# Optimization experiments

Hardware: AMD Instinct MI355X
Metric: run time of the kernel (lower is better)

Reference implementation:

```python
import jax, jax.numpy as jnp
import numpy as np

B, I, J, C, H = 1, 384, 384, 128, 4
CH = 128          # overall hidden
HD = CH // H      # 32 per head
INF = 1000000000.0
EPS = 1e-5


def setup_inputs() -> dict:
    key = jax.random.key(0)
    ks = jax.random.split(key, 10)
    s = 0.02
    return {
        "x": jax.random.normal(ks[0], (B, I, J, C), dtype=jnp.float32),
        "mask": jnp.ones((B, I, J), dtype=jnp.float32),
        "ln_w": jnp.ones((C,), dtype=jnp.float32),
        "ln_b": jnp.zeros((C,), dtype=jnp.float32),
        "wz": jax.random.normal(ks[1], (C, H), dtype=jnp.float32) * s,
        "bz": jnp.zeros((H,), dtype=jnp.float32),
        "wq": jax.random.normal(ks[2], (C, CH), dtype=jnp.float32) * s,
        "wk": jax.random.normal(ks[3], (C, CH), dtype=jnp.float32) * s,
        "wv": jax.random.normal(ks[4], (C, CH), dtype=jnp.float32) * s,
        "wg": jax.random.normal(ks[5], (C, CH), dtype=jnp.float32) * s,
        "bg": jnp.ones((CH,), dtype=jnp.float32),
        "wo": jax.random.normal(ks[6], (CH, C), dtype=jnp.float32) * s,
        "bo": jnp.zeros((C,), dtype=jnp.float32),
    }


def _layer_norm(x, w, b):
    mu = jnp.mean(x, axis=-1, keepdims=True)
    var = jnp.mean(jnp.square(x - mu), axis=-1, keepdims=True)
    return (x - mu) * jax.lax.rsqrt(var + EPS) * w + b


def reference(x, mask, ln_w, ln_b, wz, bz, wq, wk, wv, wg, bg, wo, bo):
    # starting=True: attention over last row axis J
    x = _layer_norm(x, ln_w, ln_b)                      # [B,I,J,C]
    mask_bias = (INF * (mask - 1.0))[:, :, None, None, :]   # [B,I,1,1,J]
    # triangle bias: linear_z then permute (2,0,1), unsqueeze(-4) -> [B,1,H,I,J]
    tri_bias = jnp.einsum("bijc,ch->bhij", x, wz) + bz[None, :, None, None]
    tri_bias = tri_bias[:, None]                        # [B,1,H,I,J]

    q = jnp.einsum("bijc,cd->bijd", x, wq).reshape(B, I, J, H, HD)
    k = jnp.einsum("bijc,cd->bijd", x, wk).reshape(B, I, J, H, HD)
    v = jnp.einsum("bijc,cd->bijd", x, wv).reshape(B, I, J, H, HD)
    q = q / jnp.sqrt(jnp.float32(HD))

    a = jnp.einsum("biqhd,bikhd->bihqk", q, k)          # [B,I,H,J,J]
    a = a + mask_bias + tri_bias
    a = jax.nn.softmax(a, axis=-1)
    o = jnp.einsum("bihqk,bikhd->biqhd", a, v)          # [B,I,J,H,HD]

    g = jax.nn.sigmoid(jnp.einsum("bijc,cd->bijd", x, wg) + bg)
    o = o.reshape(B, I, J, CH) * g
    return jnp.einsum("bijd,dc->bijc", o, wo) + bo      # [B,I,J,C]
```

## Files before the change

### kernel.cpp

```cpp
#include <hip/hip_runtime.h>
#include <math.h>

#define I_DIM 384
#define C_DIM 128
#define H_NUM 4
#define HD_DIM 32
#define M_DIM (I_DIM*I_DIM)
#define INF_F 1000000000.0f
#define EPS_F 1e-5f
#define QSCALE 0.17677669529663687f
#define LOG2E_F 1.4426950408889634f

typedef __attribute__((ext_vector_type(8))) short short8;
typedef __attribute__((ext_vector_type(4))) float f32x4;
union U4S8 { uint4 u; short8 s; };

__device__ __forceinline__ unsigned short f2bf(float f) {
    unsigned int u = __float_as_uint(f);
    u += 0x7fffu + ((u >> 16) & 1u);
    return (unsigned short)(u >> 16);
}
__device__ __forceinline__ float bf2f(unsigned short h) {
    return __uint_as_float((unsigned int)h << 16);
}
__device__ __forceinline__ unsigned int pk2(float a, float b) {
    return (unsigned int)f2bf(a) | ((unsigned int)f2bf(b) << 16);
}
__device__ __forceinline__ unsigned int cvtpk(float lo, float hi) {
    unsigned int r;
    asm("v_cvt_pk_bf16_f32 %0, %1, %2" : "=v"(r) : "v"(lo), "v"(hi));
    return r;
}

__device__ uint4 wfmt_dev[5*4096];

__device__ __forceinline__ void load_lds16(const uint4* gp, void* lp) {
    __builtin_amdgcn_global_load_lds(
        (const __attribute__((address_space(1))) unsigned int*)gp,
        (__attribute__((address_space(3))) unsigned int*)lp,
        16, 0, 0);
}

__global__ __launch_bounds__(256) void wprep_kernel(
    const float* __restrict__ wq, const float* __restrict__ wk,
    const float* __restrict__ wg, const float* __restrict__ wv,
    const float* __restrict__ wo)
{
    const int tid  = blockIdx.x*256 + threadIdx.x;
    const int l    = tid & 63, tile = tid >> 6;
    const int ks   = tile & 3, nt = (tile >> 2) & 7;
    const int s    = (tile >> 5) & 1, m = tile >> 6;
    const float* W = (m==0)?wq:(m==1)?wk:(m==2)?wg:(m==3)?wv:wo;
    const float scale = (m==0) ? QSCALE*LOG2E_F : 1.f;
    const int n  = nt*16 + (l & 15);
    const int kb = ks*32 + (l >> 4)*8;
    unsigned int hw[4];
    #pragma unroll
    for (int jp = 0; jp < 4; ++jp) {
        unsigned short hs[2];
        #pragma unroll
        for (int e = 0; e < 2; ++e) {
            float v = W[(size_t)(kb + jp*2 + e)*C_DIM + n] * scale;
            unsigned short h = f2bf(v);
            if (s) h = f2bf(v - bf2f(h));
            hs[e] = h;
        }
        hw[jp] = (unsigned int)hs[0] | ((unsigned int)hs[1] << 16);
    }
    wfmt_dev[(size_t)m*4096 + (size_t)((s*8 + nt)*4 + ks)*64 + l] =
        make_uint4(hw[0], hw[1], hw[2], hw[3]);
}

__global__ __launch_bounds__(256, 3) void ln_proj_kernel(
    const float* __restrict__ x,
    const float* __restrict__ lnw, const float* __restrict__ lnb,
    const float* __restrict__ wz,  const float* __restrict__ bz,
    const float* __restrict__ bg,
    float* __restrict__ qo, unsigned short* __restrict__ ko16,
    unsigned int* __restrict__ vto, float* __restrict__ go,
    float* __restrict__ zo)
{
    __shared__ __align__(16) unsigned int xs[4096];
    __shared__ __align__(16) uint4 wbuf4[2048];
    unsigned int* vts = xs;

    const int t    = threadIdx.x;
    const int row0 = blockIdx.x * 64;
    const int w = t >> 6, l = t & 63, n16 = l & 15, quad = l >> 4;

    #pragma unroll
    for (int it = 0; it < 4; ++it) {
        const int tl = w*4 + it;
        const int s = tl >> 3, ntl = (tl >> 2) & 1, ks = tl & 3;
        load_lds16(wfmt_dev + (size_t)((s*8 + ntl)*4 + ks)*64 + l,
                   (char*)wbuf4 + tl*1024);
    }

    float4 xv[8];
    const int r = t >> 2, qt = t & 3, c0 = qt * 32;
    const int sw = (r & 7) << 2;
    {
        const float* xrow = x + (size_t)(row0 + r)*C_DIM + c0;
        float s = 0.f, ss = 0.f;
        #pragma unroll
        for (int i2 = 0; i2 < 8; i2++) {
            xv[i2] = ((const float4*)xrow)[i2];
            s  += xv[i2].x + xv[i2].y + xv[i2].z + xv[i2].w;
            ss += xv[i2].x*xv[i2].x + xv[i2].y*xv[i2].y
                + xv[i2].z*xv[i2].z + xv[i2].w*xv[i2].w;
        }
        s  += __shfl_xor(s, 1);  s  += __shfl_xor(s, 2);
        ss += __shfl_xor(ss, 1); ss += __shfl_xor(ss, 2);
        const float mean = s * (1.f/128.f);
        const float var  = ss * (1.f/128.f) - mean*mean;
        const float rstd = rsqrtf(var + EPS_F);
        const float4* wz4 = (const float4*)wz;
        float4 zacc = make_float4(0.f,0.f,0.f,0.f);
        #pragma unroll
        for (int i2 = 0; i2 < 8; i2++) {
            float4 w4 = ((const float4*)(lnw + c0))[i2];
            float4 b4 = ((const float4*)(lnb + c0))[i2];
            float4 r4;
            r4.x = (xv[i2].x - mean)*rstd*w4.x + b4.x;
            r4.y = (xv[i2].y - mean)*rstd*w4.y + b4.y;
            r4.z = (xv[i2].z - mean)*rstd*w4.z + b4.z;
            r4.w = (xv[i2].w - mean)*rstd*w4.w + b4.w;
            const float4 za = wz4[c0 + i2*4 + 0];
            const float4 zb_ = wz4[c0 + i2*4 + 1];
            const float4 zc = wz4[c0 + i2*4 + 2];
            const float4 zd = wz4[c0 + i2*4 + 3];
            zacc.x += r4.x*za.x + r4.y*zb_.x + r4.z*zc.x + r4.w*zd.x;
            zacc.y += r4.x*za.y + r4.y*zb_.y + r4.z*zc.y + r4.w*zd.y;
            zacc.z += r4.x*za.z + r4.y*zb_.z + r4.z*zc.z + r4.w*zd.z;
            zacc.w += r4.x*za.w + r4.y*zb_.w + r4.z*zc.w + r4.w*zd.w;
            const int wi = r*64 + qt*16 + i2*2;
            xs[(wi  ) ^ sw] = pk2(r4.x, r4.y);
            xs[(wi+1) ^ sw] = pk2(r4.z, r4.w);
            xv[i2] = r4;
        }
        zacc.x += __shfl_xor(zacc.x, 1); zacc.x += __shfl_xor(zacc.x, 2);
        zacc.y += __shfl_xor(zacc.y, 1); zacc.y += __shfl_xor(zacc.y, 2);
        zacc.z += __shfl_xor(zacc.z, 1); zacc.z += __shfl_xor(zacc.z, 2);
        zacc.w += __shfl_xor(zacc.w, 1); zacc.w += __shfl_xor(zacc.w, 2);
        const float zv = (qt==0)?zacc.x:(qt==1)?zacc.y:(qt==2)?zacc.z:zacc.w;
        zo[(size_t)qt*M_DIM + row0 + r] = (zv + bz[qt]) * LOG2E_F;
    }
    __syncthreads();

    U4S8 ah[4], al[4];
    const int arow = w*16 + n16;
    #pragma unroll
    for (int ks = 0; ks < 4; ++ks) {
        const int bofs = arow*256 + ((ks*64 + quad*16) ^ ((arow & 7) << 4));
        ah[ks].u = *(const uint4*)((const char*)xs + bofs);
    }
    __syncthreads();

    #pragma unroll
    for (int i2 = 0; i2 < 8; i2++) {
        const float4 r4 = xv[i2];
        const unsigned short h0 = f2bf(r4.x), h1 = f2bf(r4.y),
                             h2 = f2bf(r4.z), h3 = f2bf(r4.w);
        const int wi = r*64 + qt*16 + i2*2;
        xs[(wi  ) ^ sw] = (unsigned int)f2bf(r4.x - bf2f(h0))
                        | ((unsigned int)f2bf(r4.y - bf2f(h1)) << 16);
        xs[(wi+1) ^ sw] = (unsigned int)f2bf(r4.z - bf2f(h2))
                        | ((unsigned int)f2bf(r4.w - bf2f(h3)) << 16);
    }
    __syncthreads();
    #pragma unroll
    for (int ks = 0; ks < 4; ++ks) {
        const int bofs = arow*256 + ((ks*64 + quad*16) ^ ((arow & 7) << 4));
        al[ks].u = *(const uint4*)((const char*)xs + bofs);
    }

    const int i_blk = row0 / I_DIM;
    const int jp0   = (row0 % I_DIM) >> 1;
    const int rw0   = row0 + w*16 + quad*4;

    int p = 0;
    #pragma unroll
    for (int rd = 0; rd < 16; ++rd) {
        const int mi = rd >> 2, qq = rd & 3;

        if (rd < 15) {
            const int m2 = (rd+1) >> 2, q2 = (rd+1) & 3;
            #pragma unroll
            for (int it = 0; it < 4; ++it) {
                const int tl = w*4 + it;
                const int s = tl >> 3, ntl2 = (tl >> 2) & 1, ks = tl & 3;
                load_lds16(wfmt_dev + (size_t)m2*4096
                           + (size_t)((s*8 + (q2*2 + ntl2))*4 + ks)*64 + l,
                           (char*)wbuf4 + (p^1)*16384 + tl*1024);
            }
        }

        f32x4 acc[2];
        #pragma unroll
        for (int ntl = 0; ntl < 2; ++ntl) {
            f32x4 a = {0.f, 0.f, 0.f, 0.f};
            #pragma unroll
            for (int ks = 0; ks < 4; ++ks) {
                U4S8 bh, bl;
                bh.u = wbuf4[p*1024 + (    ntl*4 + ks)*64 + l];
                bl.u = wbuf4[p*1024 + (8 + ntl*4 + ks)*64 + l];
                a = __builtin_amdgcn_mfma_f32_16x16x32_bf16(ah[ks].s, bh.s, a, 0,0,0);
                a = __builtin_amdgcn_mfma_f32_16x16x32_bf16(al[ks].s, bh.s, a, 0,0,0);
                a = __builtin_amdgcn_mfma_f32_16x16x32_bf16(ah[ks].s, bl.s, a, 0,0,0);
            }
            acc[ntl] = a;
        }

        if (mi == 0) {
            #pragma unroll
            for (int ntl = 0; ntl < 2; ++ntl)
                #pragma unroll
                for (int rr = 0; rr < 4; ++rr)
                    qo[(size_t)(rw0 + rr)*C_DIM + qq*32 + ntl*16 + n16] =
                        acc[ntl][rr];
        } else if (mi == 1) {
            #pragma unroll
            for (int ntl = 0; ntl < 2; ++ntl)
                #pragma unroll
                for (int rr = 0; rr < 4; ++rr)
                    ko16[(size_t)(rw0 + rr)*C_DIM + qq*32 + ntl*16 + n16] =
                        f2bf(acc[ntl][rr]);
        } else if (mi == 2) {
            #pragma unroll
            for (int ntl = 0; ntl < 2; ++ntl) {
                const float bgv = bg[qq*32 + ntl*16 + n16];
                #pragma unroll
                for (int rr = 0; rr < 4; ++rr)
                    go[(size_t)(rw0 + rr)*C_DIM + qq*32 + ntl*16 + n16] =
                        1.f/(1.f + __expf(-(acc[ntl][rr] + bgv)));
            }
        } else {
            #pragma unroll
            for (int ntl = 0; ntl < 2; ++ntl)
                #pragma unroll
                for (int pr = 0; pr < 2; ++pr)
                    vts[(ntl*16 + n16)*33 + w*8 + quad*2 + pr] =
                        pk2(acc[ntl][2*pr], acc[ntl][2*pr+1]);
            __syncthreads();
            for (int idx = t; idx < 32*32; idx += 256) {
                const int ch_l = idx >> 5, pp = idx & 31;
                vto[((size_t)i_blk*C_DIM + qq*32 + ch_l)*192 + jp0 + pp] =
                    vts[ch_l*33 + pp];
            }
        }

        __syncthreads();
        p ^= 1;
    }
}

__global__ __launch_bounds__(256, 4) void attn_mfma_kernel(
    const float* q, const unsigned short* __restrict__ k16,
    const unsigned int* __restrict__ vt32, const float* __restrict__ zb,
    const float* __restrict__ mask, float* o)
{
    __shared__ uint4 VTf[24*64];
    __shared__ __align__(16) float mbl[384];

    const int ii = blockIdx.x;
    const int h  = blockIdx.y;
    const int t  = threadIdx.x;
    const size_t rbase = (size_t)ii*I_DIM*C_DIM + h*HD_DIM;

    for (int idx = t; idx < 1536; idx += 256) {
        const int d = idx / 48, m = idx - d*48;
        const int c = m / 12, rr = m - c*12;
        const int km = rr >> 2, qd = rr & 3;
        const int hh = d >> 4, nn = d & 15;
        const int f  = (c*3 + km)*2 + hh;
        const int l0 = qd*16 + nn;
        const int lp = l0 ^ ((l0 >> 3) & 7) ^ ((3*c + km) & 7);
        VTf[f*64 + lp] =
            ((const uint4*)vt32)[((size_t)ii*C_DIM + h*HD_DIM + d)*48 + m];
    }
    for (int jj = t; jj < 384; jj += 256)
        mbl[jj] = (INF_F*LOG2E_F) * (mask[(size_t)ii*I_DIM + jj] - 1.f);
    __syncthreads();

    const int w = t >> 6, l = t & 63;
    const int n16 = l & 15, quad = l >> 4;
    const int slA = n16 + ((quad & 1) << 5);
    const int slB = slA + 16;
    const bool hi = (quad & 2) != 0;
    const int lswz = l ^ ((l >> 3) & 7);
    const unsigned short* kf = k16 + rbase + (size_t)n16*C_DIM + quad*8;

    #pragma unroll 1
    for (int qt = 0; qt < 6; qt++) {
        const int qg = w*6 + qt;

        U4S8 a;
        {
            const float* qrow = q + rbase + (size_t)(qg*16 + n16)*C_DIM + quad*8;
            const float4 f0 = ((const float4*)qrow)[0];
            const float4 f1 = ((const float4*)qrow)[1];
            a.u = make_uint4(cvtpk(f0.x,f0.y), cvtpk(f0.z,f0.w),
                             cvtpk(f1.x,f1.y), cvtpk(f1.z,f1.w));
        }

        f32x4 oacc0 = {0.f,0.f,0.f,0.f}, oacc1 = {0.f,0.f,0.f,0.f};
        float lsum = 0.f;
        const float* zrow = zb + (size_t)h*M_DIM
                          + (size_t)(qg*16 + n16)*I_DIM + quad*4;

        #pragma unroll 1
        for (int c = 0; c < 4; c++) {
            U4S8 kb[6];
            #pragma unroll
            for (int k6 = 0; k6 < 6; k6++)
                kb[k6].u = *(const uint4*)(kf + (size_t)((6*c + k6)*16)*C_DIM);
            float4 zc4[6];
            #pragma unroll
            for (int k6 = 0; k6 < 6; k6++)
                zc4[k6] = *(const float4*)&zrow[96*c + k6*16];
            float4 mb4[6];
            #pragma unroll
            for (int k6 = 0; k6 < 6; k6++)
                mb4[k6] = *(const float4*)&mbl[96*c + k6*16 + quad*4];

            f32x4 accS[6];
            #pragma unroll
            for (int k6 = 0; k6 < 6; k6++)
                accS[k6] = __builtin_amdgcn_mfma_f32_16x16x32_bf16(
                    kb[k6].s, a.s, (f32x4){0.f,0.f,0.f,0.f}, 0, 0, 0);

            unsigned int pu[6][2];
            #pragma unroll
            for (int k6 = 0; k6 < 6; k6++) {
                const float e0 = __builtin_amdgcn_exp2f(accS[k6][0] + zc4[k6].x + mb4[k6].x);
                const float e1 = __builtin_amdgcn_exp2f(accS[k6][1] + zc4[k6].y + mb4[k6].y);
                const float e2 = __builtin_amdgcn_exp2f(accS[k6][2] + zc4[k6].z + mb4[k6].z);
                const float e3 = __builtin_amdgcn_exp2f(accS[k6][3] + zc4[k6].w + mb4[k6].w);
                lsum += (e0 + e1) + (e2 + e3);
                pu[k6][0] = cvtpk(e0, e1);
                pu[k6][1] = cvtpk(e2, e3);
            }

            #pragma unroll
            for (int km = 0; km < 3; km++) {
                const unsigned int x0 = __shfl((int)pu[2*km  ][0], slA);
                const unsigned int x1 = __shfl((int)pu[2*km+1][0], slA);
                const unsigned int y0 = __shfl((int)pu[2*km  ][1], slA);
                const unsigned int y1 = __shfl((int)pu[2*km+1][1], slA);
                const unsigned int z0 = __shfl((int)pu[2*km  ][0], slB);
                const unsigned int z1 = __shfl((int)pu[2*km+1][0], slB);
                const unsigned int w0 = __shfl((int)pu[2*km  ][1], slB);
                const unsigned int w1 = __shfl((int)pu[2*km+1][1], slB);
                U4S8 pa;
                pa.u = make_uint4(hi?x1:x0, hi?y1:y0, hi?z1:z0, hi?w1:w0);
                const int mix = (3*c + km) & 7;
                U4S8 vb0, vb1;
                vb0.u = VTf[((c*3 + km)*2    )*64 + (lswz ^ mix)];
                vb1.u = VTf[((c*3 + km)*2 + 1)*64 + (lswz ^ mix)];
                oacc0 = __builtin_amdgcn_mfma_f32_16x16x32_bf16(vb0.s, pa.s, oacc0, 0,0,0);
                oacc1 = __builtin_amdgcn_mfma_f32_16x16x32_bf16(vb1.s, pa.s, oacc1, 0,0,0);
            }
        }

        float s_ = lsum;
        s_ += __shfl_xor(s_, 16);
        s_ += __shfl_xor(s_, 32);
        const float rcp = 1.f / s_;
        const size_t orow = rbase + (size_t)(qg*16 + n16)*C_DIM;
        float4 o0 = make_float4(oacc0[0]*rcp, oacc0[1]*rcp,
                                oacc0[2]*rcp, oacc0[3]*rcp);
        float4 o1 = make_float4(oacc1[0]*rcp, oacc1[1]*rcp,
                                oacc1[2]*rcp, oacc1[3]*rcp);
        *(float4*)&o[orow + quad*4]      = o0;
        *(float4*)&o[orow + 16 + quad*4] = o1;
    }
}

__global__ __launch_bounds__(256, 3) void out_proj_kernel(
    const float* __restrict__ o, const float* g,
    const float* __restrict__ bo, float* out)
{
    __shared__ __align__(16) unsigned int xs[4096];
    __shared__ __align__(16) uint4 wbuf4[2048];
    const int t    = threadIdx.x;
    const int row0 = blockIdx.x * 64;
    const int w = t >> 6, l = t & 63, n16 = l & 15, quad = l >> 4;

    #pragma unroll
    for (int it = 0; it < 4; ++it) {
        const int tl = w*4 + it;
        const int s = tl >> 3, ntl = (tl >> 2) & 1, ks = tl & 3;
        load_lds16(wfmt_dev + (size_t)4*4096 + (size_t)((s*8 + ntl)*4 + ks)*64 + l,
                   (char*)wbuf4 + tl*1024);
    }

    float4 pv[8];
    const int r = t >> 2, qt = t & 3, c0 = qt * 32;
    const int sw = (r & 7) << 2;
    {
        const float4* orow = (const float4*)(o + (size_t)(row0 + r)*C_DIM + c0);
        const float4* grow = (const float4*)(g + (size_t)(row0 + r)*C_DIM + c0);
        #pragma unroll
        for (int i2 = 0; i2 < 8; i2++) {
            const float4 a = orow[i2];
            const float4 b = grow[i2];
            float4 p;
            p.x = a.x*b.x; p.y = a.y*b.y; p.z = a.z*b.z; p.w = a.w*b.w;
            const int wi = r*64 + qt*16 + i2*2;
            xs[(wi  ) ^ sw] = pk2(p.x, p.y);
            xs[(wi+1) ^ sw] = pk2(p.z, p.w);
            pv[i2] = p;
        }
    }
    __syncthreads();

    U4S8 ah[4], al[4];
    const int arow = w*16 + n16;
    #pragma unroll
    for (int ks = 0; ks < 4; ++ks) {
        const int bofs = arow*256 + ((ks*64 + quad*16) ^ ((arow & 7) << 4));
        ah[ks].u = *(const uint4*)((const char*)xs + bofs);
    }
    __syncthreads();
    #pragma unroll
    for (int i2 = 0; i2 < 8; i2++) {
        const float4 p = pv[i2];
        const unsigned short h0 = f2bf(p.x), h1 = f2bf(p.y),
                             h2 = f2bf(p.z), h3 = f2bf(p.w);
        const int wi = r*64 + qt*16 + i2*2;
        xs[(wi  ) ^ sw] = (unsigned int)f2bf(p.x - bf2f(h0))
                        | ((unsigned int)f2bf(p.y - bf2f(h1)) << 16);
        xs[(wi+1) ^ sw] = (unsigned int)f2bf(p.z - bf2f(h2))
                        | ((unsigned int)f2bf(p.w - bf2f(h3)) << 16);
    }
    __syncthreads();
    #pragma unroll
    for (int ks = 0; ks < 4; ++ks) {
        const int bofs = arow*256 + ((ks*64 + quad*16) ^ ((arow & 7) << 4));
        al[ks].u = *(const uint4*)((const char*)xs + bofs);
    }

    const int rw0 = row0 + w*16 + quad*4;
    int p = 0;
    #pragma unroll
    for (int qq = 0; qq < 4; ++qq) {
        if (qq < 3) {
            const int q2 = qq + 1;
            #pragma unroll
            for (int it = 0; it < 4; ++it) {
                const int tl = w*4 + it;
                const int s = tl >> 3, ntl2 = (tl >> 2) & 1, ks = tl & 3;
                load_lds16(wfmt_dev + (size_t)4*4096
                           + (size_t)((s*8 + (q2*2 + ntl2))*4 + ks)*64 + l,
                           (char*)wbuf4 + (p^1)*16384 + tl*1024);
            }
        }
        f32x4 acc[2];
        #pragma unroll
        for (int ntl = 0; ntl < 2; ++ntl) {
            f32x4 a = {0.f, 0.f, 0.f, 0.f};
            #pragma unroll
            for (int ks = 0; ks < 4; ++ks) {
                U4S8 bh, bl;
                bh.u = wbuf4[p*1024 + (    ntl*4 + ks)*64 + l];
                bl.u = wbuf4[p*1024 + (8 + ntl*4 + ks)*64 + l];
                a = __builtin_amdgcn_mfma_f32_16x16x32_bf16(ah[ks].s, bh.s, a, 0,0,0);
                a = __builtin_amdgcn_mfma_f32_16x16x32_bf16(al[ks].s, bh.s, a, 0,0,0);
                a = __builtin_amdgcn_mfma_f32_16x16x32_bf16(ah[ks].s, bl.s, a, 0,0,0);
            }
            acc[ntl] = a;
        }
        #pragma unroll
        for (int ntl = 0; ntl < 2; ++ntl) {
            const int n = qq*32 + ntl*16 + n16;
            const float bov = bo[n];
            #pragma unroll
            for (int rr = 0; rr < 4; ++rr)
                out[(size_t)(rw0 + rr)*C_DIM + n] = acc[ntl][rr] + bov;
        }
        __syncthreads();
        p ^= 1;
    }
}

extern "C" void kernel_launch(void* const* d_in, const int* in_sizes, int n_in,
                              void* d_out, int out_size, void* d_ws, size_t ws_size,
                              hipStream_t stream)
{
    (void)in_sizes; (void)n_in; (void)out_size; (void)ws_size;
    const float* x    = (const float*)d_in[0];
    const float* mask = (const float*)d_in[1];
    const float* lnw  = (const float*)d_in[2];
    const float* lnb  = (const float*)d_in[3];
    const float* wz   = (const float*)d_in[4];
    const float* bz   = (const float*)d_in[5];
    const float* wq   = (const float*)d_in[6];
    const float* wk   = (const float*)d_in[7];
    const float* wv   = (const float*)d_in[8];
    const float* wg   = (const float*)d_in[9];
    const float* bg   = (const float*)d_in[10];
    const float* wo   = (const float*)d_in[11];
    const float* bo   = (const float*)d_in[12];

    float* ws = (float*)d_ws;
    float* qb   = ws;
    float* zbuf = qb + (size_t)M_DIM*C_DIM;
    unsigned short* kb16 = (unsigned short*)(zbuf + (size_t)H_NUM*M_DIM);
    unsigned int*   vt32 = (unsigned int*)(kb16 + (size_t)M_DIM*C_DIM);
    float* gbuf = (float*)d_out;

    wprep_kernel<<<80, 256, 0, stream>>>(wq, wk, wg, wv, wo);
    ln_proj_kernel<<<M_DIM/64, 256, 0, stream>>>(
        x, lnw, lnb, wz, bz, bg, qb, kb16, vt32, gbuf, zbuf);
    attn_mfma_kernel<<<dim3(I_DIM, H_NUM), 256, 0, stream>>>(
        qb, kb16, vt32, zbuf, mask, qb );
    out_proj_kernel<<<M_DIM/64, 256, 0, stream>>>(
        qb, gbuf, bo, (float*)d_out);
}
```

Measured before the change: 511.6 us.

## Stage K tile in LDS with XOR swizzle and pad V tile layout

The attention kernel now copies the block's whole K slice (384 keys x 32 dims, bf16) into shared memory with an XOR swizzle and reads MFMA B operands from LDS, instead of each wave loading K from global memory on every query tile. The V transpose buffer switches from the XOR-swizzled fragment layout to a simple padded row layout (stride 49). Launch bounds drop from 4 to 3 blocks per CU to fit the extra 24KB of shared memory. The aim is to cut repeated global/L2 traffic for K across the four waves and six query tiles, at the cost of lower occupancy and possible LDS bank conflicts.

```diff
diff --git a/kernel.cpp b/kernel.cpp
--- a/kernel.cpp
+++ b/kernel.cpp
@@ -254,12 +254,13 @@
     }
 }
 
-__global__ __launch_bounds__(256, 4) void attn_mfma_kernel(
+__global__ __launch_bounds__(256, 3) void attn_mfma_kernel(
     const float* q, const unsigned short* __restrict__ k16,
     const unsigned int* __restrict__ vt32, const float* __restrict__ zb,
     const float* __restrict__ mask, float* o)
 {
-    __shared__ uint4 VTf[24*64];
+    __shared__ uint4 Ks4[384*4];
+    __shared__ uint4 VTl[32*49];
     __shared__ __align__(16) float mbl[384];
 
     const int ii = blockIdx.x;
@@ -268,15 +269,13 @@
     const size_t rbase = (size_t)ii*I_DIM*C_DIM + h*HD_DIM;
 
     for (int idx = t; idx < 1536; idx += 256) {
+        const int j = idx >> 2, c4 = idx & 3;
+        Ks4[j*4 + (c4 ^ ((j >> 1) & 3))] =
+            ((const uint4*)k16)[rbase/8 + (size_t)j*16 + c4];
+    }
+    for (int idx = t; idx < 1536; idx += 256) {
         const int d = idx / 48, m = idx - d*48;
-        const int c = m / 12, rr = m - c*12;
-        const int km = rr >> 2, qd = rr & 3;
-        const int hh = d >> 4, nn = d & 15;
-        const int f  = (c*3 + km)*2 + hh;
-        const int l0 = qd*16 + nn;
-        const int lp = l0 ^ ((l0 >> 3) & 7) ^ ((3*c + km) & 7);
-        VTf[f*64 + lp] =
-            ((const uint4*)vt32)[((size_t)ii*C_DIM + h*HD_DIM + d)*48 + m];
+        VTl[d*49 + m] = ((const uint4*)vt32)[((size_t)ii*C_DIM + h*HD_DIM + d)*48 + m];
     }
     for (int jj = t; jj < 384; jj += 256)
         mbl[jj] = (INF_F*LOG2E_F) * (mask[(size_t)ii*I_DIM + jj] - 1.f);
@@ -287,8 +286,6 @@
     const int slA = n16 + ((quad & 1) << 5);
     const int slB = slA + 16;
     const bool hi = (quad & 2) != 0;
-    const int lswz = l ^ ((l >> 3) & 7);
-    const unsigned short* kf = k16 + rbase + (size_t)n16*C_DIM + quad*8;
 
     #pragma unroll 1
     for (int qt = 0; qt < 6; qt++) {
@@ -310,10 +307,6 @@
 
         #pragma unroll 1
         for (int c = 0; c < 4; c++) {
-            U4S8 kb[6];
-            #pragma unroll
-            for (int k6 = 0; k6 < 6; k6++)
-                kb[k6].u = *(const uint4*)(kf + (size_t)((6*c + k6)*16)*C_DIM);
             float4 zc4[6];
             #pragma unroll
             for (int k6 = 0; k6 < 6; k6++)
@@ -325,9 +318,13 @@
 
             f32x4 accS[6];
             #pragma unroll
-            for (int k6 = 0; k6 < 6; k6++)
+            for (int k6 = 0; k6 < 6; k6++) {
+                const int key = (6*c + k6)*16 + n16;
+                U4S8 b;
+                b.u = Ks4[key*4 + (quad ^ ((key >> 1) & 3))];
                 accS[k6] = __builtin_amdgcn_mfma_f32_16x16x32_bf16(
-                    kb[k6].s, a.s, (f32x4){0.f,0.f,0.f,0.f}, 0, 0, 0);
+                    b.s, a.s, (f32x4){0.f,0.f,0.f,0.f}, 0, 0, 0);
+            }
 
             unsigned int pu[6][2];
             #pragma unroll
@@ -353,10 +350,9 @@
                 const unsigned int w1 = __shfl((int)pu[2*km+1][1], slB);
                 U4S8 pa;
                 pa.u = make_uint4(hi?x1:x0, hi?y1:y0, hi?z1:z0, hi?w1:w0);
-                const int mix = (3*c + km) & 7;
                 U4S8 vb0, vb1;
-                vb0.u = VTf[((c*3 + km)*2    )*64 + (lswz ^ mix)];
-                vb1.u = VTf[((c*3 + km)*2 + 1)*64 + (lswz ^ mix)];
+                vb0.u = VTl[(n16     )*49 + quad + 4*km + 12*c];
+                vb1.u = VTl[(16 + n16)*49 + quad + 4*km + 12*c];
                 oacc0 = __builtin_amdgcn_mfma_f32_16x16x32_bf16(vb0.s, pa.s, oacc0, 0,0,0);
                 oacc1 = __builtin_amdgcn_mfma_f32_16x16x32_bf16(vb1.s, pa.s, oacc1, 0,0,0);
             }
```

After: 435.9 us. 1.17x faster.
